# Kernel tuning notes

Measured on AMD Instinct MI355X. Metric: run time of the kernel, lower is better.

## Reference

```python
import jax, jax.numpy as jnp
import numpy as np

B, NB, DIM, R = 4096, 64, 512, 4
INTER = DIM // R
EPS = 1e-5


def setup_inputs() -> dict:
    key = jax.random.key(0)
    ks = jax.random.split(key, 14)
    inp = {
        "t": jax.random.normal(ks[0], (B, NB, DIM), dtype=jnp.float32),
        # branch 1: Conv1d(dim->inter, k=1) == per-branch linear
        "W1": jax.random.normal(ks[1], (NB, INTER, DIM), dtype=jnp.float32) * 0.02,
        "b1": jax.random.normal(ks[2], (NB, INTER), dtype=jnp.float32) * 0.02,
        "g1": 1.0 + 0.1 * jax.random.normal(ks[3], (NB, INTER), dtype=jnp.float32),
        "beta1": 0.1 * jax.random.normal(ks[4], (NB, INTER), dtype=jnp.float32),
        "m1": 0.1 * jax.random.normal(ks[5], (NB, INTER), dtype=jnp.float32),
        "v1": jax.random.uniform(ks[6], (NB, INTER), dtype=jnp.float32, minval=0.5, maxval=1.5),
        # branch 2: Conv1d(inter->dim, k=1)
        "W2": jax.random.normal(ks[7], (NB, DIM, INTER), dtype=jnp.float32) * 0.02,
        "b2": jax.random.normal(ks[8], (NB, DIM), dtype=jnp.float32) * 0.02,
        "g2": 1.0 + 0.1 * jax.random.normal(ks[9], (NB, DIM), dtype=jnp.float32),
        "beta2": 0.1 * jax.random.normal(ks[10], (NB, DIM), dtype=jnp.float32),
        "m2": 0.1 * jax.random.normal(ks[11], (NB, DIM), dtype=jnp.float32),
        "v2": jax.random.uniform(ks[12], (NB, DIM), dtype=jnp.float32, minval=0.5, maxval=1.5),
    }
    return inp


def reference(t, W1, b1, g1, beta1, m1, v1, W2, b2, g2, beta2, m2, v2):
    # t: (B, nb, dim). torch: t.transpose(1,2).sum(-1) -> sum over nb axis.
    s = t.sum(axis=1)  # (B, dim)
    # All nb branches batched as one grouped GEMM: h = relu(BN1(W1 @ s + b1))
    h = jnp.einsum('nid,bd->bni', W1, s) + b1  # (B, nb, inter)
    h = (h - m1) * jax.lax.rsqrt(v1 + EPS) * g1 + beta1
    h = jax.nn.relu(h)
    y = jnp.einsum('ndi,bni->bnd', W2, h) + b2  # (B, nb, dim)
    y = (y - m2) * jax.lax.rsqrt(v2 + EPS) * g2 + beta2
    w = jax.nn.sigmoid(y)  # (B, nb, dim)
    # r = sum_j w[:, j, :] * t[:, j, :] * 3
    return (w * t).sum(axis=1) * 3.0  # (B, dim)
```

## Files before the change

### kernel.cpp

```cpp
#include <hip/hip_runtime.h>

#define B_SZ  4096
#define NB    64
#define DIM   512
#define INTER 128
#define EPSV  1e-5f

using f32x4  = __attribute__((ext_vector_type(4))) float;
using bf16x8 = __attribute__((ext_vector_type(8))) __bf16;
using short8 = __attribute__((ext_vector_type(8))) short;

static __device__ __forceinline__ unsigned short f2bf(float f) {
    union { float f; unsigned u; } v; v.f = f;
    return (unsigned short)((v.u + 0x7fffu + ((v.u >> 16) & 1u)) >> 16);
}

static __device__ __forceinline__ f32x4 mfma16(short8 a, short8 b, f32x4 c) {
    return __builtin_amdgcn_mfma_f32_16x16x32_bf16(
        __builtin_bit_cast(bf16x8, a), __builtin_bit_cast(bf16x8, b), c, 0, 0, 0);
}

__global__ void prep_kernel(
    const float4* __restrict__ W1, const float4* __restrict__ W2,
    const float* __restrict__ b1, const float* __restrict__ g1,
    const float* __restrict__ beta1, const float* __restrict__ m1,
    const float* __restrict__ v1,
    const float* __restrict__ b2, const float* __restrict__ g2,
    const float* __restrict__ beta2, const float* __restrict__ m2,
    const float* __restrict__ v2,
    ushort4* __restrict__ w1bf, ushort4* __restrict__ w2bf,
    float* __restrict__ sc1, float* __restrict__ bi1,
    float* __restrict__ sc2, float* __restrict__ bi2)
{
    int idx = blockIdx.x * blockDim.x + threadIdx.x;
    float4 a = W1[idx];
    ushort4 pa; pa.x = f2bf(a.x); pa.y = f2bf(a.y); pa.z = f2bf(a.z); pa.w = f2bf(a.w);
    w1bf[idx] = pa;
    float4 b = W2[idx];
    ushort4 pb; pb.x = f2bf(b.x); pb.y = f2bf(b.y); pb.z = f2bf(b.z); pb.w = f2bf(b.w);
    w2bf[idx] = pb;
    if (idx < NB * INTER) {
        float s = g1[idx] * rsqrtf(v1[idx] + EPSV);
        sc1[idx] = s;
        bi1[idx] = (b1[idx] - m1[idx]) * s + beta1[idx];
    }
    if (idx < NB * DIM) {
        float s = g2[idx] * rsqrtf(v2[idx] + EPSV);
        sc2[idx] = s;
        bi2[idx] = (b2[idx] - m2[idx]) * s + beta2[idx];
    }
}

__global__ void sum_kernel(const float* __restrict__ t, unsigned short* __restrict__ sbf)
{
    int tid = threadIdx.x;
    int b = blockIdx.x * 2 + (tid >> 7);
    int c = tid & 127;
    const float4* tb = (const float4*)t + (size_t)b * (NB * DIM / 4) + c;
    float4 acc = tb[0];
    for (int n = 1; n < NB; ++n) {
        float4 v = tb[n * (DIM / 4)];
        acc.x += v.x; acc.y += v.y; acc.z += v.z; acc.w += v.w;
    }
    ushort4 o; o.x = f2bf(acc.x); o.y = f2bf(acc.y); o.z = f2bf(acc.z); o.w = f2bf(acc.w);
    ((ushort4*)sbf)[(size_t)b * 128 + c] = o;
}

__global__ void zero_kernel(float4* __restrict__ out)
{
    out[blockIdx.x * 256 + threadIdx.x] = (float4){0.f, 0.f, 0.f, 0.f};
}

__global__ __launch_bounds__(256) void gemm1_kernel(
    const unsigned short* __restrict__ sbf,
    const unsigned short* __restrict__ w1bf,
    const float* __restrict__ sc1, const float* __restrict__ bi1,
    unsigned short* __restrict__ h)
{
    const int btile = blockIdx.x;
    const int n     = blockIdx.y;
    const int tid  = threadIdx.x;
    const int w    = tid >> 6;
    const int lane = tid & 63;
    const int quad = lane >> 4;
    const int l16  = lane & 15;
    const int m0 = btile * 128 + (w & 1) * 64;
    const int i0 = (w >> 1) * 64;

    f32x4 acc[4][4];
    #pragma unroll
    for (int a = 0; a < 4; ++a)
        #pragma unroll
        for (int c = 0; c < 4; ++c) acc[a][c] = (f32x4){0.f, 0.f, 0.f, 0.f};

    const unsigned short* w1n = w1bf + (size_t)n * (INTER * DIM);
    const unsigned short* abase = sbf + (size_t)(m0 + l16) * DIM + (quad << 3);
    const unsigned short* bbase = w1n + (size_t)(i0 + l16) * DIM + (quad << 3);

    #pragma unroll 2
    for (int s = 0; s < 16; ++s) {
        short8 af[4], bf[4];
        #pragma unroll
        for (int a = 0; a < 4; ++a)
            af[a] = *(const short8*)(abase + (size_t)(a * 16) * DIM + s * 32);
        #pragma unroll
        for (int c = 0; c < 4; ++c)
            bf[c] = *(const short8*)(bbase + (size_t)(c * 16) * DIM + s * 32);
        #pragma unroll
        for (int a = 0; a < 4; ++a)
            #pragma unroll
            for (int c = 0; c < 4; ++c)
                acc[a][c] = mfma16(af[a], bf[c], acc[a][c]);
    }

    unsigned short* hn = h + (size_t)n * (B_SZ * INTER);
    #pragma unroll
    for (int c = 0; c < 4; ++c) {
        const int i = i0 + c * 16 + l16;
        const float sc = sc1[n * INTER + i];
        const float bi = bi1[n * INTER + i];
        #pragma unroll
        for (int a = 0; a < 4; ++a) {
            #pragma unroll
            for (int r = 0; r < 4; ++r) {
                const int m = m0 + a * 16 + quad * 4 + r;
                float v = acc[a][c][r] * sc + bi;
                v = v > 0.f ? v : 0.f;
                hn[(size_t)m * INTER + i] = f2bf(v);
            }
        }
    }
}

__global__ __launch_bounds__(256) void gemm2_kernel(
    const float* __restrict__ t,
    const unsigned short* __restrict__ h,
    const unsigned short* __restrict__ w2bf,
    const float* __restrict__ sc2, const float* __restrict__ bi2,
    float* __restrict__ out)
{
    const int btile = blockIdx.x;
    const int dtile = blockIdx.y;
    const int ng    = blockIdx.z;
    const int tid  = threadIdx.x;
    const int w    = tid >> 6;
    const int lane = tid & 63;
    const int quad = lane >> 4;
    const int l16  = lane & 15;
    const int d0 = dtile * 64;

    f32x4 oacc[4];
    #pragma unroll
    for (int c = 0; c < 4; ++c) oacc[c] = (f32x4){0.f, 0.f, 0.f, 0.f};

    const unsigned short* habase =
        h + (size_t)(btile * 64 + w * 16 + l16) * INTER + (quad << 3);

    for (int n = ng * 32; n < ng * 32 + 32; ++n) {
        const unsigned short* hn  = habase + (size_t)n * (B_SZ * INTER);
        const unsigned short* w2n = w2bf + (size_t)n * (DIM * INTER)
                                  + (size_t)(d0 + l16) * INTER + (quad << 3);
        f32x4 yacc[4];
        #pragma unroll
        for (int c = 0; c < 4; ++c) yacc[c] = (f32x4){0.f, 0.f, 0.f, 0.f};

        #pragma unroll
        for (int s = 0; s < 4; ++s) {
            short8 af = *(const short8*)(hn + s * 32);
            #pragma unroll
            for (int c = 0; c < 4; ++c) {
                short8 bf = *(const short8*)(w2n + (size_t)(c * 16) * INTER + s * 32);
                yacc[c] = mfma16(af, bf, yacc[c]);
            }
        }

        #pragma unroll
        for (int c = 0; c < 4; ++c) {
            const int d = d0 + c * 16 + l16;
            const float sc = sc2[n * DIM + d];
            const float bi = bi2[n * DIM + d];
            #pragma unroll
            for (int r = 0; r < 4; ++r) {
                const int m = btile * 64 + w * 16 + quad * 4 + r;
                float y  = yacc[c][r] * sc + bi;
                float wv = 1.f / (1.f + __expf(-y));
                float tv = t[((size_t)m * NB + n) * DIM + d];
                oacc[c][r] += wv * tv;
            }
        }
    }

    #pragma unroll
    for (int c = 0; c < 4; ++c) {
        const int d = d0 + c * 16 + l16;
        #pragma unroll
        for (int r = 0; r < 4; ++r) {
            const int m = btile * 64 + w * 16 + quad * 4 + r;
            unsafeAtomicAdd(&out[(size_t)m * DIM + d], oacc[c][r] * 3.0f);
        }
    }
}

extern "C" void kernel_launch(void* const* d_in, const int* in_sizes, int n_in,
                              void* d_out, int out_size, void* d_ws, size_t ws_size,
                              hipStream_t stream)
{
    const float* t     = (const float*)d_in[0];
    const float* W1    = (const float*)d_in[1];
    const float* b1    = (const float*)d_in[2];
    const float* g1    = (const float*)d_in[3];
    const float* beta1 = (const float*)d_in[4];
    const float* m1    = (const float*)d_in[5];
    const float* v1    = (const float*)d_in[6];
    const float* W2    = (const float*)d_in[7];
    const float* b2    = (const float*)d_in[8];
    const float* g2    = (const float*)d_in[9];
    const float* beta2 = (const float*)d_in[10];
    const float* m2    = (const float*)d_in[11];
    const float* v2    = (const float*)d_in[12];

    char* ws = (char*)d_ws;
    unsigned short* w1bf = (unsigned short*)(ws);
    unsigned short* w2bf = (unsigned short*)(ws + 8388608);
    unsigned short* sbf  = (unsigned short*)(ws + 16777216);
    float* sc1 = (float*)(ws + 20971520);
    float* bi1 = (float*)(ws + 21004288);
    float* sc2 = (float*)(ws + 21037056);
    float* bi2 = (float*)(ws + 21168128);
    unsigned short* hbuf = (unsigned short*)(ws + 21299200);

    prep_kernel<<<4096, 256, 0, stream>>>(
        (const float4*)W1, (const float4*)W2,
        b1, g1, beta1, m1, v1, b2, g2, beta2, m2, v2,
        (ushort4*)w1bf, (ushort4*)w2bf, sc1, bi1, sc2, bi2);

    sum_kernel<<<2048, 256, 0, stream>>>(t, sbf);

    zero_kernel<<<2048, 256, 0, stream>>>((float4*)d_out);

    gemm1_kernel<<<dim3(32, 64), 256, 0, stream>>>(sbf, w1bf, sc1, bi1, hbuf);

    gemm2_kernel<<<dim3(64, 8, 2), 256, 0, stream>>>(t, hbuf, w2bf, sc2, bi2, (float*)d_out);
}
```

Before: 1.205 ms.

## Transpose gemm2 MFMA operands for vectorized t loads; split branches and sum reduction wider

In gemm2 the MFMA operands are swapped so each lane holds four consecutive d values for one batch row. The t, sc2 and bi2 loads become float4 and are issued before the MFMA. The branch split grows from 2 to 4 groups, doubling the grid but also the number of atomic adds into the output. The sum kernel now uses one block per batch row, with two thread halves each reducing 32 branches and then combining through shared memory, which adds more parallelism to that pass.

Result: slower. 1.274 ms (+5.7%).

```diff
diff --git a/kernel.cpp b/kernel.cpp
--- a/kernel.cpp
+++ b/kernel.cpp
@@ -53,17 +53,28 @@
 
 __global__ void sum_kernel(const float* __restrict__ t, unsigned short* __restrict__ sbf)
 {
-    int tid = threadIdx.x;
-    int b = blockIdx.x * 2 + (tid >> 7);
-    int c = tid & 127;
+    const int b = blockIdx.x;
+    const int g = threadIdx.x >> 7;
+    const int c = threadIdx.x & 127;
     const float4* tb = (const float4*)t + (size_t)b * (NB * DIM / 4) + c;
-    float4 acc = tb[0];
-    for (int n = 1; n < NB; ++n) {
-        float4 v = tb[n * (DIM / 4)];
+
+    float4 acc = {0.f, 0.f, 0.f, 0.f};
+    #pragma unroll 8
+    for (int i = 0; i < 32; ++i) {
+        float4 v = tb[(size_t)(g * 32 + i) * (DIM / 4)];
         acc.x += v.x; acc.y += v.y; acc.z += v.z; acc.w += v.w;
     }
-    ushort4 o; o.x = f2bf(acc.x); o.y = f2bf(acc.y); o.z = f2bf(acc.z); o.w = f2bf(acc.w);
-    ((ushort4*)sbf)[(size_t)b * 128 + c] = o;
+
+    __shared__ float4 red[128];
+    if (g) red[c] = acc;
+    __syncthreads();
+    if (!g) {
+        float4 o = red[c];
+        acc.x += o.x; acc.y += o.y; acc.z += o.z; acc.w += o.w;
+        ushort4 st; st.x = f2bf(acc.x); st.y = f2bf(acc.y);
+        st.z = f2bf(acc.z); st.w = f2bf(acc.w);
+        ((ushort4*)sbf)[(size_t)b * 128 + c] = st;
+    }
 }
 
 __global__ void zero_kernel(float4* __restrict__ out)
@@ -148,16 +159,27 @@
     const int quad = lane >> 4;
     const int l16  = lane & 15;
     const int d0 = dtile * 64;
+    const int m  = btile * 64 + w * 16 + l16;
 
     f32x4 oacc[4];
     #pragma unroll
     for (int c = 0; c < 4; ++c) oacc[c] = (f32x4){0.f, 0.f, 0.f, 0.f};
 
-    const unsigned short* habase =
-        h + (size_t)(btile * 64 + w * 16 + l16) * INTER + (quad << 3);
-
-    for (int n = ng * 32; n < ng * 32 + 32; ++n) {
-        const unsigned short* hn  = habase + (size_t)n * (B_SZ * INTER);
+    const unsigned short* hb = h + (size_t)m * INTER + (quad << 3);
+    const float* tb = t + (size_t)m * (NB * DIM) + d0 + quad * 4;
+
+    for (int n = ng * 16; n < ng * 16 + 16; ++n) {
+        float4 tv[4];
+        #pragma unroll
+        for (int c = 0; c < 4; ++c)
+            tv[c] = *(const float4*)(tb + (size_t)n * DIM + c * 16);
+
+        short8 bh[4];
+        const unsigned short* hn = hb + (size_t)n * (B_SZ * INTER);
+        #pragma unroll
+        for (int s = 0; s < 4; ++s)
+            bh[s] = *(const short8*)(hn + s * 32);
+
         const unsigned short* w2n = w2bf + (size_t)n * (DIM * INTER)
                                   + (size_t)(d0 + l16) * INTER + (quad << 3);
         f32x4 yacc[4];
@@ -165,39 +187,37 @@
         for (int c = 0; c < 4; ++c) yacc[c] = (f32x4){0.f, 0.f, 0.f, 0.f};
 
         #pragma unroll
-        for (int s = 0; s < 4; ++s) {
-            short8 af = *(const short8*)(hn + s * 32);
-            #pragma unroll
-            for (int c = 0; c < 4; ++c) {
-                short8 bf = *(const short8*)(w2n + (size_t)(c * 16) * INTER + s * 32);
-                yacc[c] = mfma16(af, bf, yacc[c]);
+        for (int c = 0; c < 4; ++c) {
+            #pragma unroll
+            for (int s = 0; s < 4; ++s) {
+                short8 aw = *(const short8*)(w2n + (size_t)(c * 16) * INTER + s * 32);
+                yacc[c] = mfma16(aw, bh[s], yacc[c]);
             }
         }
 
         #pragma unroll
         for (int c = 0; c < 4; ++c) {
-            const int d = d0 + c * 16 + l16;
-            const float sc = sc2[n * DIM + d];
-            const float bi = bi2[n * DIM + d];
+            const int d = d0 + c * 16 + quad * 4;
+            float4 sc = *(const float4*)(sc2 + n * DIM + d);
+            float4 bi = *(const float4*)(bi2 + n * DIM + d);
             #pragma unroll
             for (int r = 0; r < 4; ++r) {
-                const int m = btile * 64 + w * 16 + quad * 4 + r;
-                float y  = yacc[c][r] * sc + bi;
+                float scr = (r == 0) ? sc.x : (r == 1) ? sc.y : (r == 2) ? sc.z : sc.w;
+                float bir = (r == 0) ? bi.x : (r == 1) ? bi.y : (r == 2) ? bi.z : bi.w;
+                float tvr = (r == 0) ? tv[c].x : (r == 1) ? tv[c].y : (r == 2) ? tv[c].z : tv[c].w;
+                float y  = yacc[c][r] * scr + bir;
                 float wv = 1.f / (1.f + __expf(-y));
-                float tv = t[((size_t)m * NB + n) * DIM + d];
-                oacc[c][r] += wv * tv;
+                oacc[c][r] += wv * tvr;
             }
         }
     }
 
     #pragma unroll
     for (int c = 0; c < 4; ++c) {
-        const int d = d0 + c * 16 + l16;
-        #pragma unroll
-        for (int r = 0; r < 4; ++r) {
-            const int m = btile * 64 + w * 16 + quad * 4 + r;
-            unsafeAtomicAdd(&out[(size_t)m * DIM + d], oacc[c][r] * 3.0f);
-        }
+        const int d = d0 + c * 16 + quad * 4;
+        #pragma unroll
+        for (int r = 0; r < 4; ++r)
+            unsafeAtomicAdd(&out[(size_t)m * DIM + d + r], oacc[c][r] * 3.0f);
     }
 }
 
@@ -234,11 +254,11 @@
         b1, g1, beta1, m1, v1, b2, g2, beta2, m2, v2,
         (ushort4*)w1bf, (ushort4*)w2bf, sc1, bi1, sc2, bi2);
 
-    sum_kernel<<<2048, 256, 0, stream>>>(t, sbf);
+    sum_kernel<<<4096, 256, 0, stream>>>(t, sbf);
 
     zero_kernel<<<2048, 256, 0, stream>>>((float4*)d_out);
 
     gemm1_kernel<<<dim3(32, 64), 256, 0, stream>>>(sbf, w1bf, sc1, bi1, hbuf);
 
-    gemm2_kernel<<<dim3(64, 8, 2), 256, 0, stream>>>(t, hbuf, w2bf, sc2, bi2, (float*)d_out);
-}
+    gemm2_kernel<<<dim3(64, 8, 4), 256, 0, stream>>>(t, hbuf, w2bf, sc2, bi2, (float*)d_out);
+}
```
